# Kernel optimization log

Measured on AMD Instinct MI355X. Metric: run time of the kernel, lower is better.

## Reference

```python
import jax, jax.numpy as jnp
import numpy as np

DIM = 128
N_GNN = 3
VDW_N = 6.0
MAX_VDW = 0.0356
MIN_VDW = 0.0178
DEV_VDW_RADIUS = 0.2
DM_MIN = 0.5


def gated_gat(x, adj, W, Wb, A, gW, gb):
    # PIGNet-style GatedGAT: attention from bilinear form, gated residual
    h = x @ W + Wb                                   # [B,N,D]
    e = jnp.einsum('bjl,bkl->bjk', h @ A, h)
    e = e + jnp.swapaxes(e, 1, 2)
    att = jnp.where(adj > 0, e, -9e15)
    att = jax.nn.softmax(att, axis=-1) * adj
    hp = jax.nn.relu(jnp.einsum('bij,bjd->bid', att, h))
    coeff = jax.nn.sigmoid(jnp.concatenate([x, hp], axis=-1) @ gW + gb)  # [B,N,1]
    return coeff * x + (1.0 - coeff) * hp


def pair_mlp(lig, tgt, W1, b1, W2, b2):
    # MLP on concat([lig_i, tgt_j]) without materializing [B,L,T,2D]:
    # split W1 along its input dim (exact same math as concat @ W1)
    D = lig.shape[-1]
    pre = (jnp.einsum('bld,dk->blk', lig, W1[:D])[:, :, None, :]
           + jnp.einsum('btd,dk->btk', tgt, W1[D:])[:, None, :, :] + b1)
    h = jax.nn.relu(pre)                             # [B,L,T,D]
    return jnp.einsum('bltk,ko->blt', h, W2) + b2[0]  # [B,L,T]


def setup_inputs() -> dict:
    key = jax.random.key(0)
    ks = jax.random.split(key, 20)
    B, L, T, D = 8, 128, 512, DIM
    f32 = jnp.float32

    def adj(k, n, p):
        a = (jax.random.uniform(k, (B, n, n)) < p).astype(f32)
        a = jnp.maximum(a, jnp.swapaxes(a, 1, 2))
        return jnp.minimum(a + jnp.eye(n, dtype=f32), 1.0)

    s = 0.05
    inp = dict(
        ligand_h=jax.random.normal(ks[0], (B, L, 54), f32),
        target_h=jax.random.normal(ks[1], (B, T, 54), f32),
        ligand_adj=adj(ks[2], L, 0.10),
        target_adj=adj(ks[3], T, 0.02),
        interaction_indice=(jax.random.uniform(ks[4], (B, 3, L, T)) < 0.05).astype(f32),
        ligand_pos=jax.random.uniform(ks[5], (B, L, 3), f32) * 20.0,
        target_pos=jax.random.uniform(ks[6], (B, T, 3), f32) * 20.0,
        rotor=jnp.floor(jax.random.uniform(ks[7], (B, 1), f32) * 10.0),
        ligand_vdw_radii=jax.random.uniform(ks[8], (B, L), f32) * 0.5 + 1.5,
        target_vdw_radii=jax.random.uniform(ks[9], (B, T), f32) * 0.5 + 1.5,
        ligand_valid=jnp.ones((B, L), f32),
        target_valid=jnp.ones((B, T), f32),
        emb_W=jax.random.normal(ks[10], (54, D), f32) * s,
        gat_W=jax.random.normal(ks[11], (N_GNN, D, D), f32) * s,
        gat_Wb=jnp.zeros((N_GNN, D), f32),
        gat_A=jax.random.normal(ks[12], (N_GNN, D, D), f32) * s,
        gat_gW=jax.random.normal(ks[13], (N_GNN, 2 * D, 1), f32) * s,
        gat_gb=jnp.zeros((N_GNN, 1), f32),
        vdwA_W1=jax.random.normal(ks[14], (2 * D, D), f32) * s,
        vdwA_b1=jnp.zeros((D,), f32),
        vdwA_W2=jax.random.normal(ks[15], (D, 1), f32) * s,
        vdwA_b2=jnp.zeros((1,), f32),
        dc_W1=jax.random.normal(ks[16], (2 * D, D), f32) * s,
        dc_b1=jnp.zeros((D,), f32),
        dc_W2=jax.random.normal(ks[17], (D, 1), f32) * s,
        dc_b2=jnp.zeros((1,), f32),
        hbond_coeff=jnp.array([1.0], f32),
        metal_coeff=jnp.array([1.0], f32),
        hydrophobic_coeff=jnp.array([0.5], f32),
        rotor_coeff=jnp.array([0.5], f32),
    )
    return inp


def reference(ligand_h, target_h, ligand_adj, target_adj, interaction_indice,
              ligand_pos, target_pos, rotor, ligand_vdw_radii, target_vdw_radii,
              ligand_valid, target_valid, emb_W, gat_W, gat_Wb, gat_A, gat_gW,
              gat_gb, vdwA_W1, vdwA_b1, vdwA_W2, vdwA_b2, dc_W1, dc_b1, dc_W2,
              dc_b2, hbond_coeff, metal_coeff, hydrophobic_coeff, rotor_coeff):
    lig = ligand_h @ emb_W
    tgt = target_h @ emb_W
    # pairwise distance matrix with min-distance clamp
    diff = ligand_pos[:, :, None, :] - target_pos[:, None, :, :]
    dm = jnp.sqrt((diff * diff).sum(-1) + 1e-10)      # [B,L,T]
    dm = jnp.where(dm < DM_MIN, 1e10, dm)
    for i in range(N_GNN):  # eval mode: dropout is identity
        lig = gated_gat(lig, ligand_adj, gat_W[i], gat_Wb[i], gat_A[i], gat_gW[i], gat_gb[i])
        tgt = gated_gat(tgt, target_adj, gat_W[i], gat_Wb[i], gat_A[i], gat_gW[i], gat_gb[i])
    vdws_sum = ligand_vdw_radii[:, :, None] + target_vdw_radii[:, None, :]
    # dm_correction=True: tanh MLP on pairwise concat features, scaled by dev_vdw_radius
    vdws_sum = vdws_sum + jnp.tanh(pair_mlp(lig, tgt, dc_W1, dc_b1, dc_W2, dc_b2)) * DEV_VDW_RADIUS
    # --- vdw term ---
    dm_0 = jnp.where(vdws_sum < 1e-4, 1.0, vdws_sum)
    ratio = dm_0 / dm
    valid = ligand_valid[:, :, None] * target_valid[:, None, :]
    energy = jnp.minimum(ratio ** (2.0 * VDW_N) - 2.0 * ratio ** VDW_N, 100.0) * valid
    A = jax.nn.sigmoid(pair_mlp(lig, tgt, vdwA_W1, vdwA_b1, vdwA_W2, vdwA_b2))
    A = A * (MAX_VDW - MIN_VDW) + MIN_VDW
    vdw_e = (A * energy).sum((1, 2))                  # [B]
    # --- hbond / metal / hydrophobic ramps share dm - vdws_sum ---
    d = dm - vdws_sum
    ramp = jnp.clip(d / -0.7, 0.0, 1.0)
    hbond_e = -(hbond_coeff[0] ** 2) * (ramp * interaction_indice[:, 0]).sum((1, 2))
    metal_e = -(metal_coeff[0] ** 2) * (ramp * interaction_indice[:, 1]).sum((1, 2))
    ramp2 = jnp.clip(-d + 1.5, 0.0, 1.0)
    hydro_e = -(hydrophobic_coeff[0] ** 2) * (ramp2 * interaction_indice[:, 2]).sum((1, 2))
    energies = jnp.stack([vdw_e, hbond_e, metal_e, hydro_e], axis=-1)  # [B,4]
    energies = energies / (1.0 + rotor_coeff[0] ** 2 * rotor)          # rotor penalty
    return energies
```

## Files before the change

### kernel.cpp

```cpp
#include <hip/hip_runtime.h>
#include <hip/hip_bf16.h>
#include <math.h>

typedef __hip_bfloat16 bf16;

#define DIMD 128
#define BB 8
#define LL 128
#define TT 512

#define BMT 64
#define BKT 32
#define TGT_TILES 36
#define LIG_TILES 3

#define CV_EMBW   0L
#define CV_GATW   (CV_EMBW + 54 * 128)
#define CV_GATA   (CV_GATW + 3 * 128 * 128)
#define CV_WB     (CV_GATA + 3 * 128 * 128)
#define CV_GGW    (CV_WB + 3 * 128)
#define CV_GGB    (CV_GGW + 3 * 2 * 128)
#define CV_DCW1   (CV_GGB + 4)
#define CV_VW1    (CV_DCW1 + 2 * 128 * 128)
#define CV_TOTAL  (CV_VW1 + 2 * 128 * 128)

__device__ __forceinline__ float LD(const void* p, long i, int bf) {
    if (bf) return __bfloat162float(((const bf16*)p)[i]);
    return ((const float*)p)[i];
}

__global__ void init_cvt(const unsigned int* __restrict__ embw_raw,
                         const void* __restrict__ embW, const void* __restrict__ gatW,
                         const void* __restrict__ gatA, const void* __restrict__ gatWb,
                         const void* __restrict__ ggW, const void* __restrict__ ggb,
                         const void* __restrict__ dcW1, const void* __restrict__ vW1,
                         float* __restrict__ out, float* __restrict__ accum,
                         int* __restrict__ flagp) {
    __shared__ int cnts;
    int t = threadIdx.x;
    if (t == 0) cnts = 0;
    __syncthreads();
    unsigned int bword = (embw_raw[t] >> 8) & 0xffu;
    unsigned int e = bword & 0x7fu;
    if (e >= 0x38u && e <= 0x3fu) atomicAdd(&cnts, 1);
    __syncthreads();
    int bf = cnts > 128;
    if (blockIdx.x == 0) {
        if (t < 32) accum[t] = 0.0f;
        if (t == 0) *flagp = bf;
    }
    long i = (long)blockIdx.x * 256 + t;
    if (i >= CV_TOTAL) return;
    float v;
    if (i < CV_GATW)      v = LD(embW, i, bf);
    else if (i < CV_GATA) v = LD(gatW, i - CV_GATW, bf);
    else if (i < CV_WB)   v = LD(gatA, i - CV_GATA, bf);
    else if (i < CV_GGW)  v = LD(gatWb, i - CV_WB, bf);
    else if (i < CV_GGB)  v = LD(ggW, i - CV_GGW, bf);
    else if (i < CV_DCW1) { long j = i - CV_GGB; v = (j < 3) ? LD(ggb, j, bf) : 0.0f; }
    else if (i < CV_VW1)  v = LD(dcW1, i - CV_DCW1, bf);
    else                  v = LD(vW1, i - CV_VW1, bf);
    out[i] = v;
}

__global__ void embed_both(const void* __restrict__ Xl, const void* __restrict__ Xt,
                           const float* __restrict__ Wf, float* __restrict__ out,
                           int K, const int* __restrict__ flagp) {
    __shared__ float xrow[DIMD];
    int bf = *flagp;
    int row = blockIdx.x;
    int d = threadIdx.x;
    const void* X; long r;
    if (row < BB * LL) { X = Xl; r = row; }
    else               { X = Xt; r = row - BB * LL; }
    if (d < K) xrow[d] = LD(X, r * K + d, bf);
    __syncthreads();
    float acc = 0.0f;
    for (int k = 0; k < K; ++k)
        acc = fmaf(xrow[k], Wf[(long)k * DIMD + d], acc);
    out[(long)row * DIMD + d] = acc;
}

__global__ void gemm_hha_gate(float* __restrict__ X, const float* __restrict__ P0,
                              const float* __restrict__ P1, const float* __restrict__ cvw,
                              int layer, int dogate,
                              float* __restrict__ hout, float* __restrict__ hAout) {
    __shared__ float xs[4][DIMD];
    __shared__ float hs[4][DIMD];
    __shared__ float gred[4][2];
    long row0 = (long)blockIdx.x * 4;
    int d = threadIdx.x & 127, rg = threadIdx.x >> 7;
    int w = threadIdx.x >> 6, lane = threadIdx.x & 63;
    long r0 = row0 + rg * 2, r1 = r0 + 1;
    float xv0 = X[r0 * DIMD + d];
    float xv1 = X[r1 * DIMD + d];
    if (dogate) {
        const float* gW = cvw + CV_GGW + (long)(layer - 1) * 2 * DIMD;
        float gb = cvw[CV_GGB + (layer - 1)];
        float hp0 = fmaxf(P0[r0 * DIMD + d] + P1[r0 * DIMD + d], 0.0f);
        float hp1 = fmaxf(P0[r1 * DIMD + d] + P1[r1 * DIMD + d], 0.0f);
        float s0 = xv0 * gW[d] + hp0 * gW[DIMD + d];
        float s1 = xv1 * gW[d] + hp1 * gW[DIMD + d];
#pragma unroll
        for (int s = 32; s > 0; s >>= 1) { s0 += __shfl_xor(s0, s); s1 += __shfl_xor(s1, s); }
        if (lane == 0) { gred[rg * 2 + 0][w & 1] = s0; gred[rg * 2 + 1][w & 1] = s1; }
        __syncthreads();
        float g0 = gred[rg * 2 + 0][0] + gred[rg * 2 + 0][1] + gb;
        float g1 = gred[rg * 2 + 1][0] + gred[rg * 2 + 1][1] + gb;
        float c0 = 1.0f / (1.0f + expf(-g0));
        float c1 = 1.0f / (1.0f + expf(-g1));
        xv0 = c0 * xv0 + (1.0f - c0) * hp0;
        xv1 = c1 * xv1 + (1.0f - c1) * hp1;
        X[r0 * DIMD + d] = xv0;
        X[r1 * DIMD + d] = xv1;
    }
    xs[rg * 2 + 0][d] = xv0;
    xs[rg * 2 + 1][d] = xv1;
    __syncthreads();
    const float* W = cvw + CV_GATW + (long)layer * DIMD * DIMD;
    const float* A = cvw + CV_GATA + (long)layer * DIMD * DIMD;
    float b = cvw[CV_WB + layer * DIMD + d];
    float h0 = b, h1 = b;
    const float* x0 = xs[rg * 2];
    const float* x1 = xs[rg * 2 + 1];
#pragma unroll 8
    for (int k = 0; k < DIMD; ++k) {
        float wv = W[(long)k * DIMD + d];
        h0 = fmaf(x0[k], wv, h0);
        h1 = fmaf(x1[k], wv, h1);
    }
    long ob = r0 * DIMD + d;
    hout[ob] = h0; hout[ob + DIMD] = h1;
    hs[rg * 2][d] = h0; hs[rg * 2 + 1][d] = h1;
    __syncthreads();
    float a0 = 0.0f, a1 = 0.0f;
    const float* g0p = hs[rg * 2];
    const float* g1p = hs[rg * 2 + 1];
#pragma unroll 8
    for (int k = 0; k < DIMD; ++k) {
        float wv = A[(long)k * DIMD + d];
        a0 = fmaf(g0p[k], wv, a0);
        a1 = fmaf(g1p[k], wv, a1);
    }
    hAout[ob] = a0;
    hAout[ob + DIMD] = a1;
}

__global__ void esym_both(const float* __restrict__ hA_t, const float* __restrict__ h_t,
                          float* __restrict__ e1_t, float* __restrict__ e2_t,
                          const float* __restrict__ hA_l, const float* __restrict__ h_l,
                          float* __restrict__ e1_l, float* __restrict__ e2_l) {
    __shared__ float At[BKT][BMT + 4];
    __shared__ float Bt[BKT][BMT + 4];
    int idx = blockIdx.x, half = blockIdx.y, b = blockIdx.z, t = threadIdx.x;
    const float *hA, *h; float* e; int N;
    if (idx < TGT_TILES) { hA = hA_t; h = h_t; e = half ? e2_t : e1_t; N = TT; }
    else { idx -= TGT_TILES; hA = hA_l; h = h_l; e = half ? e2_l : e1_l; N = LL; }
    int jt = (int)((sqrtf(8.0f * idx + 1.0f) - 1.0f) * 0.5f);
    while ((jt + 1) * (jt + 2) / 2 <= idx) ++jt;
    while (jt * (jt + 1) / 2 > idx) --jt;
    int kt = idx - jt * (jt + 1) / 2;
    const float* hAb = hA + (long)b * N * DIMD;
    const float* hb  = h  + (long)b * N * DIMD;
    const float* Ap = half ? hb : hAb;
    const float* Bp = half ? hAb : hb;
    int tm = t & 15, tn = t >> 4;
    int k4 = (t & 7) * 4;
    int row0 = t >> 3;
    float acc[4][4];
#pragma unroll
    for (int i = 0; i < 4; ++i)
#pragma unroll
        for (int jj = 0; jj < 4; ++jj) acc[i][jj] = 0.0f;

#pragma unroll
    for (int c = 0; c < 4; ++c) {
        int ko = c * BKT;
        __syncthreads();
#pragma unroll
        for (int rr = 0; rr < 2; ++rr) {
            int row = row0 + rr * 32;
            float4 av = *(const float4*)&Ap[(long)(jt * BMT + row) * DIMD + ko + k4];
            float4 bv = *(const float4*)&Bp[(long)(kt * BMT + row) * DIMD + ko + k4];
            At[k4 + 0][row] = av.x; At[k4 + 1][row] = av.y;
            At[k4 + 2][row] = av.z; At[k4 + 3][row] = av.w;
            Bt[k4 + 0][row] = bv.x; Bt[k4 + 1][row] = bv.y;
            Bt[k4 + 2][row] = bv.z; Bt[k4 + 3][row] = bv.w;
        }
        __syncthreads();
#pragma unroll
        for (int k = 0; k < BKT; ++k) {
            float4 a4 = *(const float4*)&At[k][tm * 4];
            float4 b4 = *(const float4*)&Bt[k][tn * 4];
            float A[4] = {a4.x, a4.y, a4.z, a4.w};
            float Bv[4] = {b4.x, b4.y, b4.z, b4.w};
#pragma unroll
            for (int i = 0; i < 4; ++i)
#pragma unroll
                for (int jj = 0; jj < 4; ++jj)
                    acc[i][jj] = fmaf(A[i], Bv[jj], acc[i][jj]);
        }
    }
    long ebN = (long)b * N;
    long ebase = (ebN + jt * BMT + tm * 4) * N + kt * BMT + tn * 4;
#pragma unroll
    for (int i = 0; i < 4; ++i) {
        float4 v;
        v.x = acc[i][0]; v.y = acc[i][1]; v.z = acc[i][2]; v.w = acc[i][3];
        *(float4*)&e[ebase + (long)i * N] = v;
    }
    if (jt != kt) {
        long mbase = (ebN + kt * BMT + tn * 4) * N + jt * BMT + tm * 4;
#pragma unroll
        for (int jj = 0; jj < 4; ++jj) {
            float4 v;
            v.x = acc[0][jj]; v.y = acc[1][jj]; v.z = acc[2][jj]; v.w = acc[3][jj];
            *(float4*)&e[mbase + (long)jj * N] = v;
        }
    }
}

template<int CNT>
__device__ __forceinline__ void softmax_row(float* __restrict__ e1row,
                                            const float* __restrict__ e2row,
                                            const void* __restrict__ adj,
                                            long adjbase, int bf) {
    int lane = threadIdx.x & 63;
    float vals[CNT], av[CNT];
    float m = -3.4e38f;
#pragma unroll
    for (int i = 0; i < CNT; ++i) {
        int k = lane + i * 64;
        float a = LD(adj, adjbase + k, bf);
        float v = (a > 0.0f) ? (e1row[k] + e2row[k]) : -9e15f;
        av[i] = a; vals[i] = v;
        m = fmaxf(m, v);
    }
#pragma unroll
    for (int s = 32; s > 0; s >>= 1) m = fmaxf(m, __shfl_xor(m, s));
    float sum = 0.0f;
#pragma unroll
    for (int i = 0; i < CNT; ++i) { vals[i] = expf(vals[i] - m); sum += vals[i]; }
#pragma unroll
    for (int s = 32; s > 0; s >>= 1) sum += __shfl_xor(sum, s);
    float inv = 1.0f / sum;
#pragma unroll
    for (int i = 0; i < CNT; ++i)
        e1row[lane + i * 64] = vals[i] * av[i] * inv;
}

__global__ void att_softmax_both(float* __restrict__ e1_t, const float* __restrict__ e2_t,
                                 float* __restrict__ e1_l, const float* __restrict__ e2_l,
                                 const void* __restrict__ adj_t, const void* __restrict__ adj_l,
                                 const int* __restrict__ flagp) {
    int bf = *flagp;
    int b = blockIdx.y, x = blockIdx.x;
    int jr = threadIdx.x >> 6;
    if (x < TT / 4) {
        int j = x * 4 + jr;
        long base = ((long)b * TT + j) * TT;
        softmax_row<8>(e1_t + base, e2_t + base, adj_t, base, bf);
    } else {
        int j = (x - TT / 4) * 4 + jr;
        long base = ((long)b * LL + j) * LL;
        softmax_row<2>(e1_l + base, e2_l + base, adj_l, base, bf);
    }
}

__global__ void hp_gemm_both(const float* __restrict__ att_t, const float* __restrict__ h_t,
                             float* __restrict__ p0_t, float* __restrict__ p1_t,
                             const float* __restrict__ att_l, const float* __restrict__ h_l,
                             float* __restrict__ p0_l, float* __restrict__ p1_l) {
    __shared__ float At[32][36];
    __shared__ float Ht[32][DIMD];
    int jt = blockIdx.x, kc = blockIdx.y, b = blockIdx.z;
    int t = threadIdx.x;
    const float *att, *h; float *part0, *part1; int N;
    if (jt < 16) { att = att_t; h = h_t; part0 = p0_t; part1 = p1_t; N = TT; }
    else { jt -= 16; att = att_l; h = h_l; part0 = p0_l; part1 = p1_l; N = LL; }
    const float* attb = att + (long)b * N * N;
    const float* hb = h + (long)b * N * DIMD;
    int tm = t & 7, tn = t >> 3;
    float acc[4][4] = {};
    int kchunk = N / 2;
    int kbeg = kc * kchunk;
    int ar = t >> 3;
    int ac4 = (t & 7) * 4;
    int hk = t >> 5;
    int hc4 = (t & 31) * 4;
    for (int k0 = kbeg; k0 < kbeg + kchunk; k0 += 32) {
        __syncthreads();
        float4 av = *(const float4*)&attb[(long)(jt * 32 + ar) * N + k0 + ac4];
        At[ac4 + 0][ar] = av.x; At[ac4 + 1][ar] = av.y;
        At[ac4 + 2][ar] = av.z; At[ac4 + 3][ar] = av.w;
#pragma unroll
        for (int p = 0; p < 4; ++p)
            *(float4*)&Ht[hk + p * 8][hc4] = *(const float4*)&hb[(long)(k0 + hk + p * 8) * DIMD + hc4];
        __syncthreads();
#pragma unroll
        for (int k = 0; k < 32; ++k) {
            float4 a4 = *(const float4*)&At[k][tm * 4];
            float4 h4 = *(const float4*)&Ht[k][tn * 4];
            float A[4] = {a4.x, a4.y, a4.z, a4.w};
            float H[4] = {h4.x, h4.y, h4.z, h4.w};
#pragma unroll
            for (int i = 0; i < 4; ++i)
#pragma unroll
                for (int jj = 0; jj < 4; ++jj)
                    acc[i][jj] = fmaf(A[i], H[jj], acc[i][jj]);
        }
    }
    float* outp = (kc == 0) ? part0 : part1;
    long obase = ((long)b * N + jt * 32 + tm * 4) * DIMD + tn * 4;
#pragma unroll
    for (int i = 0; i < 4; ++i) {
        float4 v; v.x = acc[i][0]; v.y = acc[i][1]; v.z = acc[i][2]; v.w = acc[i][3];
        *(float4*)&outp[obase + (long)i * DIMD] = v;
    }
}

__global__ void proj_gate(const float* __restrict__ X, const float* __restrict__ P0,
                          const float* __restrict__ P1, const float* __restrict__ cvw,
                          const void* __restrict__ bdc, const void* __restrict__ bA,
                          long rowsplit, float* __restrict__ outdc, float* __restrict__ outA,
                          const int* __restrict__ flagp) {
    __shared__ float xs[4][DIMD];
    __shared__ float gred[4][2];
    int bf = *flagp;
    long row0 = (long)blockIdx.x * 4;
    int d = threadIdx.x & 127, rg = threadIdx.x >> 7;
    int w = threadIdx.x >> 6, lane = threadIdx.x & 63;
    long r0 = row0 + rg * 2, r1 = r0 + 1;
    float xv0 = X[r0 * DIMD + d];
    float xv1 = X[r1 * DIMD + d];
    {
        const float* gW = cvw + CV_GGW + 2L * 2 * DIMD;
        float gb = cvw[CV_GGB + 2];
        float hp0 = fmaxf(P0[r0 * DIMD + d] + P1[r0 * DIMD + d], 0.0f);
        float hp1 = fmaxf(P0[r1 * DIMD + d] + P1[r1 * DIMD + d], 0.0f);
        float s0 = xv0 * gW[d] + hp0 * gW[DIMD + d];
        float s1 = xv1 * gW[d] + hp1 * gW[DIMD + d];
#pragma unroll
        for (int s = 32; s > 0; s >>= 1) { s0 += __shfl_xor(s0, s); s1 += __shfl_xor(s1, s); }
        if (lane == 0) { gred[rg * 2 + 0][w & 1] = s0; gred[rg * 2 + 1][w & 1] = s1; }
        __syncthreads();
        float g0 = gred[rg * 2 + 0][0] + gred[rg * 2 + 0][1] + gb;
        float g1 = gred[rg * 2 + 1][0] + gred[rg * 2 + 1][1] + gb;
        float c0 = 1.0f / (1.0f + expf(-g0));
        float c1 = 1.0f / (1.0f + expf(-g1));
        xv0 = c0 * xv0 + (1.0f - c0) * hp0;
        xv1 = c1 * xv1 + (1.0f - c1) * hp1;
    }
    xs[rg * 2 + 0][d] = xv0;
    xs[rg * 2 + 1][d] = xv1;
    __syncthreads();
    const float* Wf = (blockIdx.y == 0) ? (cvw + CV_DCW1) : (cvw + CV_VW1);
    const void* bias = (blockIdx.y == 0) ? bdc : bA;
    float* out = (blockIdx.y == 0) ? outdc : outA;
    int sideb = row0 >= rowsplit;
    const float* W = Wf + (sideb ? (long)DIMD * DIMD : 0);
    float b0 = sideb ? 0.0f : LD(bias, d, bf);
    float a0 = b0, a1 = b0;
    const float* x0 = xs[rg * 2];
    const float* x1 = xs[rg * 2 + 1];
#pragma unroll 8
    for (int k = 0; k < DIMD; ++k) {
        float wv = W[(long)k * DIMD + d];
        a0 = fmaf(x0[k], wv, a0);
        a1 = fmaf(x1[k], wv, a1);
    }
    long ob = r0 * DIMD + d;
    out[ob] = a0;
    out[ob + DIMD] = a1;
}

__global__ void transpose_both(const float* __restrict__ in0, float* __restrict__ out0,
                               const float* __restrict__ in1, float* __restrict__ out1) {
    __shared__ float tile[32][33];
    int z = blockIdx.z;
    const float* in; float* outT; int b;
    if (z < BB) { in = in0; outT = out0; b = z; }
    else        { in = in1; outT = out1; b = z - BB; }
    int n0 = blockIdx.x * 32;
    int d0 = blockIdx.y * 32;
    int t = threadIdx.x;
    int tx = t & 31, ty = t >> 5;
    for (int r = ty; r < 32; r += 8)
        tile[r][tx] = in[((long)b * TT + n0 + r) * DIMD + d0 + tx];
    __syncthreads();
    for (int r = ty; r < 32; r += 8)
        outT[((long)b * DIMD + d0 + r) * TT + n0 + tx] = tile[tx][r];
}

__global__ void pair_energy(const float* __restrict__ ligdc, const float* __restrict__ tgtdcT,
                            const float* __restrict__ ligA, const float* __restrict__ tgtAT,
                            const void* __restrict__ dcW2, const void* __restrict__ dcb2,
                            const void* __restrict__ AW2, const void* __restrict__ Ab2,
                            const void* __restrict__ lpos, const void* __restrict__ tpos,
                            const void* __restrict__ lrad, const void* __restrict__ trad,
                            const void* __restrict__ lval, const void* __restrict__ tval,
                            const void* __restrict__ ii, float* __restrict__ accum,
                            const int* __restrict__ flagp) {
    int bf = *flagp;
    int l0 = blockIdx.x * 2, b = blockIdx.z, t = threadIdx.x;
    int tt = blockIdx.y * 256 + t;
    __shared__ __align__(16) float sdc0[DIMD], sdc1[DIMD], sA0[DIMD], sA1[DIMD];
    __shared__ __align__(16) float w2dc[DIMD], w2A[DIMD];
    __shared__ float red[256];
    if (t < DIMD) {
        sdc0[t] = ligdc[((long)b * LL + l0) * DIMD + t];
        sA0[t]  = ligA [((long)b * LL + l0) * DIMD + t];
        w2dc[t] = LD(dcW2, t, bf);
        w2A[t]  = LD(AW2, t, bf);
    } else {
        int u = t - DIMD;
        sdc1[u] = ligdc[((long)b * LL + l0 + 1) * DIMD + u];
        sA1[u]  = ligA [((long)b * LL + l0 + 1) * DIMD + u];
    }
    __syncthreads();
    const float* tdT = tgtdcT + (long)b * DIMD * TT;
    const float* taT = tgtAT  + (long)b * DIMD * TT;
    float adc0 = 0.0f, adc1 = 0.0f, aA0 = 0.0f, aA1 = 0.0f;
    for (int i4 = 0; i4 < DIMD; i4 += 4) {
#pragma unroll
        for (int j = 0; j < 4; ++j) {
            float td = tdT[(long)(i4 + j) * TT + tt];
            float ta = taT[(long)(i4 + j) * TT + tt];
            float wd = w2dc[i4 + j], wa = w2A[i4 + j];
            adc0 = fmaf(fmaxf(td + sdc0[i4 + j], 0.0f), wd, adc0);
            adc1 = fmaf(fmaxf(td + sdc1[i4 + j], 0.0f), wd, adc1);
            aA0  = fmaf(fmaxf(ta + sA0[i4 + j],  0.0f), wa, aA0);
            aA1  = fmaf(fmaxf(ta + sA1[i4 + j],  0.0f), wa, aA1);
        }
    }
    float lx0 = LD(lpos, ((long)b * LL + l0) * 3 + 0, bf);
    float ly0 = LD(lpos, ((long)b * LL + l0) * 3 + 1, bf);
    float lz0 = LD(lpos, ((long)b * LL + l0) * 3 + 2, bf);
    float lx1 = LD(lpos, ((long)b * LL + l0 + 1) * 3 + 0, bf);
    float ly1 = LD(lpos, ((long)b * LL + l0 + 1) * 3 + 1, bf);
    float lz1 = LD(lpos, ((long)b * LL + l0 + 1) * 3 + 2, bf);
    float lr0 = LD(lrad, (long)b * LL + l0, bf);
    float lr1 = LD(lrad, (long)b * LL + l0 + 1, bf);
    float lv0 = LD(lval, (long)b * LL + l0, bf);
    float lv1 = LD(lval, (long)b * LL + l0 + 1, bf);
    float cdcb2 = LD(dcb2, 0, bf), cab2 = LD(Ab2, 0, bf);
    long iiA0 = ((long)(b * 3 + 0) * LL + l0) * TT;
    long iiB0 = ((long)(b * 3 + 1) * LL + l0) * TT;
    long iiC0 = ((long)(b * 3 + 2) * LL + l0) * TT;
    long iiA1 = iiA0 + TT, iiB1 = iiB0 + TT, iiC1 = iiC0 + TT;
    float tx = LD(tpos, ((long)b * TT + tt) * 3 + 0, bf);
    float ty = LD(tpos, ((long)b * TT + tt) * 3 + 1, bf);
    float tz = LD(tpos, ((long)b * TT + tt) * 3 + 2, bf);
    float tr = LD(trad, (long)b * TT + tt, bf);
    float tv = LD(tval, (long)b * TT + tt, bf);
    float p0 = 0.0f, p1 = 0.0f, p2 = 0.0f, p3 = 0.0f;
#pragma unroll
    for (int li = 0; li < 2; ++li) {
        float dx = (li ? lx1 : lx0) - tx;
        float dy = (li ? ly1 : ly0) - ty;
        float dz = (li ? lz1 : lz0) - tz;
        float dm = sqrtf(dx * dx + dy * dy + dz * dz + 1e-10f);
        if (dm < 0.5f) dm = 1e10f;
        float adcv = li ? adc1 : adc0;
        float aAv  = li ? aA1  : aA0;
        float dev = tanhf(adcv + cdcb2) * 0.2f;
        float vdws = (li ? lr1 : lr0) + tr + dev;
        float dm0 = (vdws < 1e-4f) ? 1.0f : vdws;
        float ratio = dm0 / dm;
        float r2 = ratio * ratio, r6 = r2 * r2 * r2, r12 = r6 * r6;
        float en = fminf(r12 - 2.0f * r6, 100.0f) * (li ? lv1 : lv0) * tv;
        float As = 1.0f / (1.0f + expf(-(aAv + cab2)));
        As = As * (0.0356f - 0.0178f) + 0.0178f;
        p0 = fmaf(As, en, p0);
        float dd = dm - vdws;
        float ramp = fminf(fmaxf(dd * (1.0f / -0.7f), 0.0f), 1.0f);
        p1 = fmaf(ramp, LD(ii, (li ? iiA1 : iiA0) + tt, bf), p1);
        p2 = fmaf(ramp, LD(ii, (li ? iiB1 : iiB0) + tt, bf), p2);
        float ramp2 = fminf(fmaxf(-dd + 1.5f, 0.0f), 1.0f);
        p3 = fmaf(ramp2, LD(ii, (li ? iiC1 : iiC0) + tt, bf), p3);
    }
    for (int e = 0; e < 4; ++e) {
        float v = (e == 0) ? p0 : (e == 1) ? p1 : (e == 2) ? p2 : p3;
        red[t] = v; __syncthreads();
        for (int s = 128; s > 0; s >>= 1) { if (t < s) red[t] += red[t + s]; __syncthreads(); }
        if (t == 0) atomicAdd(&accum[b * 4 + e], red[0]);
        __syncthreads();
    }
}

__global__ void finalize(const float* __restrict__ accum, const void* __restrict__ hb,
                         const void* __restrict__ mc, const void* __restrict__ hyd,
                         const void* __restrict__ rc, const void* __restrict__ rotor,
                         void* __restrict__ out, const int* __restrict__ flagp) {
    int bf = *flagp;
    int t = threadIdx.x;
    if (t >= 32) return;
    int b = t >> 2, e = t & 3;
    float v = accum[t];
    if (e == 1) { float c = LD(hb, 0, bf);  v = -c * c * v; }
    else if (e == 2) { float c = LD(mc, 0, bf);  v = -c * c * v; }
    else if (e == 3) { float c = LD(hyd, 0, bf); v = -c * c * v; }
    float r = LD(rc, 0, bf);
    float den = 1.0f + r * r * LD(rotor, b, bf);
    float res = v / den;
    if (bf) ((bf16*)out)[t] = __float2bfloat16(res);
    else    ((float*)out)[t] = res;
}

extern "C" void kernel_launch(void* const* d_in, const int* in_sizes, int n_in,
                              void* d_out, int out_size, void* d_ws, size_t ws_size,
                              hipStream_t stream) {
    const void* ligand_h = d_in[0];
    const void* target_h = d_in[1];
    const void* ligand_adj = d_in[2];
    const void* target_adj = d_in[3];
    const void* interaction_indice = d_in[4];
    const void* ligand_pos = d_in[5];
    const void* target_pos = d_in[6];
    const void* rotor = d_in[7];
    const void* ligand_vdw = d_in[8];
    const void* target_vdw = d_in[9];
    const void* ligand_valid = d_in[10];
    const void* target_valid = d_in[11];
    const void* emb_W = d_in[12];
    const void* gat_W = d_in[13];
    const void* gat_Wb = d_in[14];
    const void* gat_A = d_in[15];
    const void* gat_gW = d_in[16];
    const void* gat_gb = d_in[17];
    const void* vdwA_W1 = d_in[18];
    const void* vdwA_b1 = d_in[19];
    const void* vdwA_W2 = d_in[20];
    const void* vdwA_b2 = d_in[21];
    const void* dc_W1 = d_in[22];
    const void* dc_b1 = d_in[23];
    const void* dc_W2 = d_in[24];
    const void* dc_b2 = d_in[25];
    const void* hbond_coeff = d_in[26];
    const void* metal_coeff = d_in[27];
    const void* hydrophobic_coeff = d_in[28];
    const void* rotor_coeff = d_in[29];

    float* ws = (float*)d_ws;
    size_t off = 0;
    float* lig_x = ws + off;  off += (size_t)BB * LL * DIMD;
    float* tgt_x = ws + off;  off += (size_t)BB * TT * DIMD;
    float* h_lig = ws + off;  off += (size_t)BB * LL * DIMD;
    float* h_tgt = ws + off;  off += (size_t)BB * TT * DIMD;
    float* hA_lig = ws + off; off += (size_t)BB * LL * DIMD;
    float* hA_tgt = ws + off; off += (size_t)BB * TT * DIMD;
    float* accum = ws + off;  off += 32;
    int* flagp = (int*)(ws + off); off += 2;
    float* e_buf = ws + off;  off += (size_t)BB * TT * TT;
    float* e_lig = ws + off;  off += (size_t)BB * LL * LL;
    float* e2_buf = ws + off; off += (size_t)BB * TT * TT;
    float* e2_lig = ws + off; off += (size_t)BB * LL * LL;
    float* part1 = ws + off;  off += (size_t)BB * (LL + TT) * DIMD;
    float* projA = ws + off;  off += (size_t)BB * (LL + TT) * DIMD;
    float* cvw   = ws + off;  off += (size_t)CV_TOTAL;
    float* part1_l = part1;
    float* part1_t = part1 + (size_t)BB * LL * DIMD;
    float* part0_lig = hA_lig;
    float* part0_tgt = hA_tgt;
    float* ligdc = h_lig;
    float* tgtdc = h_tgt;
    float* ligA = projA;
    float* tgtA = projA + (size_t)BB * LL * DIMD;
    float* tgtdcT = e_buf;
    float* tgtAT  = e_buf + (size_t)BB * DIMD * TT;
    float* wEmb = cvw + CV_EMBW;

    init_cvt<<<(CV_TOTAL + 255) / 256, 256, 0, stream>>>(
        (const unsigned int*)emb_W, emb_W, gat_W, gat_A, gat_Wb,
        gat_gW, gat_gb, dc_W1, vdwA_W1, cvw, accum, flagp);

    embed_both<<<BB * (LL + TT), DIMD, 0, stream>>>(ligand_h, target_h, wEmb, lig_x, 54, flagp);

    const long ROWSPLIT = (long)BB * LL;
    for (int i = 0; i < 3; ++i) {
        gemm_hha_gate<<<BB * (LL + TT) / 4, 256, 0, stream>>>(
            lig_x, hA_lig, part1, cvw, i, i > 0 ? 1 : 0, h_lig, hA_lig);
        esym_both<<<dim3(TGT_TILES + LIG_TILES, 2, BB), 256, 0, stream>>>(
            hA_tgt, h_tgt, e_buf, e2_buf, hA_lig, h_lig, e_lig, e2_lig);
        att_softmax_both<<<dim3(TT / 4 + LL / 4, BB), 256, 0, stream>>>(
            e_buf, e2_buf, e_lig, e2_lig, target_adj, ligand_adj, flagp);
        hp_gemm_both<<<dim3(20, 2, BB), 256, 0, stream>>>(
            e_buf, h_tgt, part0_tgt, part1_t, e_lig, h_lig, part0_lig, part1_l);
    }

    proj_gate<<<dim3(BB * (LL + TT) / 4, 2), 256, 0, stream>>>(
        lig_x, hA_lig, part1, cvw, dc_b1, vdwA_b1, ROWSPLIT, ligdc, ligA, flagp);

    transpose_both<<<dim3(TT / 32, DIMD / 32, 2 * BB), 256, 0, stream>>>(
        tgtdc, tgtdcT, tgtA, tgtAT);

    pair_energy<<<dim3(LL / 2, 2, BB), 256, 0, stream>>>(
        ligdc, tgtdcT, ligA, tgtAT, dc_W2, dc_b2, vdwA_W2, vdwA_b2,
        ligand_pos, target_pos, ligand_vdw, target_vdw,
        ligand_valid, target_valid, interaction_indice, accum, flagp);

    finalize<<<1, 64, 0, stream>>>(accum, hbond_coeff, metal_coeff,
                                   hydrophobic_coeff, rotor_coeff, rotor, d_out, flagp);
}
```

Baseline: 384.4 us.

## Split hp GEMM K four ways and restructure pair_energy tiling and reduction

The attention-times-h GEMM now splits its K dimension into four partial outputs instead of two, which doubles the grid. The gate and projection kernels sum four partials. pair_energy now has each thread handle two target columns with float2 loads and vectorised shared-memory reads, using half as many blocks. Its tree reduction through shared memory with many barriers is replaced by wave shuffles plus a small cross-wave sum. The cost is two extra partial buffers and more memory traffic when the partials are read.

```diff
diff --git a/kernel.cpp b/kernel.cpp
--- a/kernel.cpp
+++ b/kernel.cpp
@@ -82,7 +82,8 @@
 }
 
 __global__ void gemm_hha_gate(float* __restrict__ X, const float* __restrict__ P0,
-                              const float* __restrict__ P1, const float* __restrict__ cvw,
+                              const float* __restrict__ P1, const float* __restrict__ P2,
+                              const float* __restrict__ P3, const float* __restrict__ cvw,
                               int layer, int dogate,
                               float* __restrict__ hout, float* __restrict__ hAout) {
     __shared__ float xs[4][DIMD];
@@ -97,8 +98,10 @@
     if (dogate) {
         const float* gW = cvw + CV_GGW + (long)(layer - 1) * 2 * DIMD;
         float gb = cvw[CV_GGB + (layer - 1)];
-        float hp0 = fmaxf(P0[r0 * DIMD + d] + P1[r0 * DIMD + d], 0.0f);
-        float hp1 = fmaxf(P0[r1 * DIMD + d] + P1[r1 * DIMD + d], 0.0f);
+        float hp0 = fmaxf(P0[r0 * DIMD + d] + P1[r0 * DIMD + d]
+                        + P2[r0 * DIMD + d] + P3[r0 * DIMD + d], 0.0f);
+        float hp1 = fmaxf(P0[r1 * DIMD + d] + P1[r1 * DIMD + d]
+                        + P2[r1 * DIMD + d] + P3[r1 * DIMD + d], 0.0f);
         float s0 = xv0 * gW[d] + hp0 * gW[DIMD + d];
         float s1 = xv1 * gW[d] + hp1 * gW[DIMD + d];
 #pragma unroll
@@ -268,21 +271,21 @@
 }
 
 __global__ void hp_gemm_both(const float* __restrict__ att_t, const float* __restrict__ h_t,
-                             float* __restrict__ p0_t, float* __restrict__ p1_t,
                              const float* __restrict__ att_l, const float* __restrict__ h_l,
-                             float* __restrict__ p0_l, float* __restrict__ p1_l) {
+                             float* __restrict__ P0, float* __restrict__ P1,
+                             float* __restrict__ P2, float* __restrict__ P3) {
     __shared__ float At[32][36];
     __shared__ float Ht[32][DIMD];
     int jt = blockIdx.x, kc = blockIdx.y, b = blockIdx.z;
     int t = threadIdx.x;
-    const float *att, *h; float *part0, *part1; int N;
-    if (jt < 16) { att = att_t; h = h_t; part0 = p0_t; part1 = p1_t; N = TT; }
-    else { jt -= 16; att = att_l; h = h_l; part0 = p0_l; part1 = p1_l; N = LL; }
+    const float *att, *h; int N; long rowbase;
+    if (jt < 16) { att = att_t; h = h_t; N = TT; rowbase = (long)BB * LL + (long)b * TT; }
+    else { jt -= 16; att = att_l; h = h_l; N = LL; rowbase = (long)b * LL; }
     const float* attb = att + (long)b * N * N;
     const float* hb = h + (long)b * N * DIMD;
     int tm = t & 7, tn = t >> 3;
     float acc[4][4] = {};
-    int kchunk = N / 2;
+    int kchunk = N / 4;
     int kbeg = kc * kchunk;
     int ar = t >> 3;
     int ac4 = (t & 7) * 4;
@@ -310,8 +313,8 @@
                     acc[i][jj] = fmaf(A[i], H[jj], acc[i][jj]);
         }
     }
-    float* outp = (kc == 0) ? part0 : part1;
-    long obase = ((long)b * N + jt * 32 + tm * 4) * DIMD + tn * 4;
+    float* outp = (kc == 0) ? P0 : (kc == 1) ? P1 : (kc == 2) ? P2 : P3;
+    long obase = (rowbase + jt * 32 + tm * 4) * DIMD + tn * 4;
 #pragma unroll
     for (int i = 0; i < 4; ++i) {
         float4 v; v.x = acc[i][0]; v.y = acc[i][1]; v.z = acc[i][2]; v.w = acc[i][3];
@@ -320,7 +323,8 @@
 }
 
 __global__ void proj_gate(const float* __restrict__ X, const float* __restrict__ P0,
-                          const float* __restrict__ P1, const float* __restrict__ cvw,
+                          const float* __restrict__ P1, const float* __restrict__ P2,
+                          const float* __restrict__ P3, const float* __restrict__ cvw,
                           const void* __restrict__ bdc, const void* __restrict__ bA,
                           long rowsplit, float* __restrict__ outdc, float* __restrict__ outA,
                           const int* __restrict__ flagp) {
@@ -336,8 +340,10 @@
     {
         const float* gW = cvw + CV_GGW + 2L * 2 * DIMD;
         float gb = cvw[CV_GGB + 2];
-        float hp0 = fmaxf(P0[r0 * DIMD + d] + P1[r0 * DIMD + d], 0.0f);
-        float hp1 = fmaxf(P0[r1 * DIMD + d] + P1[r1 * DIMD + d], 0.0f);
+        float hp0 = fmaxf(P0[r0 * DIMD + d] + P1[r0 * DIMD + d]
+                        + P2[r0 * DIMD + d] + P3[r0 * DIMD + d], 0.0f);
+        float hp1 = fmaxf(P0[r1 * DIMD + d] + P1[r1 * DIMD + d]
+                        + P2[r1 * DIMD + d] + P3[r1 * DIMD + d], 0.0f);
         float s0 = xv0 * gW[d] + hp0 * gW[DIMD + d];
         float s1 = xv1 * gW[d] + hp1 * gW[DIMD + d];
 #pragma unroll
@@ -402,11 +408,10 @@
                             const void* __restrict__ ii, float* __restrict__ accum,
                             const int* __restrict__ flagp) {
     int bf = *flagp;
-    int l0 = blockIdx.x * 2, b = blockIdx.z, t = threadIdx.x;
-    int tt = blockIdx.y * 256 + t;
+    int l0 = blockIdx.x * 2, b = blockIdx.y, t = threadIdx.x;
     __shared__ __align__(16) float sdc0[DIMD], sdc1[DIMD], sA0[DIMD], sA1[DIMD];
     __shared__ __align__(16) float w2dc[DIMD], w2A[DIMD];
-    __shared__ float red[256];
+    __shared__ float redw[4][4];
     if (t < DIMD) {
         sdc0[t] = ligdc[((long)b * LL + l0) * DIMD + t];
         sA0[t]  = ligA [((long)b * LL + l0) * DIMD + t];
@@ -417,22 +422,27 @@
         sdc1[u] = ligdc[((long)b * LL + l0 + 1) * DIMD + u];
         sA1[u]  = ligA [((long)b * LL + l0 + 1) * DIMD + u];
     }
-    __syncthreads();
-    const float* tdT = tgtdcT + (long)b * DIMD * TT;
-    const float* taT = tgtAT  + (long)b * DIMD * TT;
-    float adc0 = 0.0f, adc1 = 0.0f, aA0 = 0.0f, aA1 = 0.0f;
-    for (int i4 = 0; i4 < DIMD; i4 += 4) {
-#pragma unroll
-        for (int j = 0; j < 4; ++j) {
-            float td = tdT[(long)(i4 + j) * TT + tt];
-            float ta = taT[(long)(i4 + j) * TT + tt];
-            float wd = w2dc[i4 + j], wa = w2A[i4 + j];
-            adc0 = fmaf(fmaxf(td + sdc0[i4 + j], 0.0f), wd, adc0);
-            adc1 = fmaf(fmaxf(td + sdc1[i4 + j], 0.0f), wd, adc1);
-            aA0  = fmaf(fmaxf(ta + sA0[i4 + j],  0.0f), wa, aA0);
-            aA1  = fmaf(fmaxf(ta + sA1[i4 + j],  0.0f), wa, aA1);
-        }
-    }
+    int tt0 = t * 2;
+    float tx0 = LD(tpos, ((long)b * TT + tt0) * 3 + 0, bf);
+    float ty0 = LD(tpos, ((long)b * TT + tt0) * 3 + 1, bf);
+    float tz0 = LD(tpos, ((long)b * TT + tt0) * 3 + 2, bf);
+    float tx1 = LD(tpos, ((long)b * TT + tt0 + 1) * 3 + 0, bf);
+    float ty1 = LD(tpos, ((long)b * TT + tt0 + 1) * 3 + 1, bf);
+    float tz1 = LD(tpos, ((long)b * TT + tt0 + 1) * 3 + 2, bf);
+    float tr0 = LD(trad, (long)b * TT + tt0, bf);
+    float tr1 = LD(trad, (long)b * TT + tt0 + 1, bf);
+    float tv0 = LD(tval, (long)b * TT + tt0, bf);
+    float tv1 = LD(tval, (long)b * TT + tt0 + 1, bf);
+    long iiA0 = ((long)(b * 3 + 0) * LL + l0) * TT;
+    long iiB0 = ((long)(b * 3 + 1) * LL + l0) * TT;
+    long iiC0 = ((long)(b * 3 + 2) * LL + l0) * TT;
+    long iiA1 = iiA0 + TT, iiB1 = iiB0 + TT, iiC1 = iiC0 + TT;
+    float iA00 = LD(ii, iiA0 + tt0, bf), iA01 = LD(ii, iiA0 + tt0 + 1, bf);
+    float iA10 = LD(ii, iiA1 + tt0, bf), iA11 = LD(ii, iiA1 + tt0 + 1, bf);
+    float iB00 = LD(ii, iiB0 + tt0, bf), iB01 = LD(ii, iiB0 + tt0 + 1, bf);
+    float iB10 = LD(ii, iiB1 + tt0, bf), iB11 = LD(ii, iiB1 + tt0 + 1, bf);
+    float iC00 = LD(ii, iiC0 + tt0, bf), iC01 = LD(ii, iiC0 + tt0 + 1, bf);
+    float iC10 = LD(ii, iiC1 + tt0, bf), iC11 = LD(ii, iiC1 + tt0 + 1, bf);
     float lx0 = LD(lpos, ((long)b * LL + l0) * 3 + 0, bf);
     float ly0 = LD(lpos, ((long)b * LL + l0) * 3 + 1, bf);
     float lz0 = LD(lpos, ((long)b * LL + l0) * 3 + 2, bf);
@@ -444,47 +454,85 @@
     float lv0 = LD(lval, (long)b * LL + l0, bf);
     float lv1 = LD(lval, (long)b * LL + l0 + 1, bf);
     float cdcb2 = LD(dcb2, 0, bf), cab2 = LD(Ab2, 0, bf);
-    long iiA0 = ((long)(b * 3 + 0) * LL + l0) * TT;
-    long iiB0 = ((long)(b * 3 + 1) * LL + l0) * TT;
-    long iiC0 = ((long)(b * 3 + 2) * LL + l0) * TT;
-    long iiA1 = iiA0 + TT, iiB1 = iiB0 + TT, iiC1 = iiC0 + TT;
-    float tx = LD(tpos, ((long)b * TT + tt) * 3 + 0, bf);
-    float ty = LD(tpos, ((long)b * TT + tt) * 3 + 1, bf);
-    float tz = LD(tpos, ((long)b * TT + tt) * 3 + 2, bf);
-    float tr = LD(trad, (long)b * TT + tt, bf);
-    float tv = LD(tval, (long)b * TT + tt, bf);
+    __syncthreads();
+    const float* tdT = tgtdcT + (long)b * DIMD * TT;
+    const float* taT = tgtAT  + (long)b * DIMD * TT;
+    float adc00 = 0.0f, adc01 = 0.0f, adc10 = 0.0f, adc11 = 0.0f;
+    float aA00 = 0.0f, aA01 = 0.0f, aA10 = 0.0f, aA11 = 0.0f;
+    for (int i4 = 0; i4 < DIMD; i4 += 4) {
+        float4 wd = *(const float4*)&w2dc[i4];
+        float4 wa = *(const float4*)&w2A[i4];
+        float4 v0d = *(const float4*)&sdc0[i4];
+        float4 v1d = *(const float4*)&sdc1[i4];
+        float4 v0a = *(const float4*)&sA0[i4];
+        float4 v1a = *(const float4*)&sA1[i4];
+        float wdv[4] = {wd.x, wd.y, wd.z, wd.w};
+        float wav[4] = {wa.x, wa.y, wa.z, wa.w};
+        float s0d[4] = {v0d.x, v0d.y, v0d.z, v0d.w};
+        float s1d[4] = {v1d.x, v1d.y, v1d.z, v1d.w};
+        float s0a[4] = {v0a.x, v0a.y, v0a.z, v0a.w};
+        float s1a[4] = {v1a.x, v1a.y, v1a.z, v1a.w};
+#pragma unroll
+        for (int j = 0; j < 4; ++j) {
+            float2 td = *(const float2*)&tdT[(long)(i4 + j) * TT + tt0];
+            float2 ta = *(const float2*)&taT[(long)(i4 + j) * TT + tt0];
+            adc00 = fmaf(fmaxf(td.x + s0d[j], 0.0f), wdv[j], adc00);
+            adc01 = fmaf(fmaxf(td.y + s0d[j], 0.0f), wdv[j], adc01);
+            adc10 = fmaf(fmaxf(td.x + s1d[j], 0.0f), wdv[j], adc10);
+            adc11 = fmaf(fmaxf(td.y + s1d[j], 0.0f), wdv[j], adc11);
+            aA00 = fmaf(fmaxf(ta.x + s0a[j], 0.0f), wav[j], aA00);
+            aA01 = fmaf(fmaxf(ta.y + s0a[j], 0.0f), wav[j], aA01);
+            aA10 = fmaf(fmaxf(ta.x + s1a[j], 0.0f), wav[j], aA10);
+            aA11 = fmaf(fmaxf(ta.y + s1a[j], 0.0f), wav[j], aA11);
+        }
+    }
     float p0 = 0.0f, p1 = 0.0f, p2 = 0.0f, p3 = 0.0f;
 #pragma unroll
-    for (int li = 0; li < 2; ++li) {
-        float dx = (li ? lx1 : lx0) - tx;
-        float dy = (li ? ly1 : ly0) - ty;
-        float dz = (li ? lz1 : lz0) - tz;
-        float dm = sqrtf(dx * dx + dy * dy + dz * dz + 1e-10f);
-        if (dm < 0.5f) dm = 1e10f;
-        float adcv = li ? adc1 : adc0;
-        float aAv  = li ? aA1  : aA0;
-        float dev = tanhf(adcv + cdcb2) * 0.2f;
-        float vdws = (li ? lr1 : lr0) + tr + dev;
-        float dm0 = (vdws < 1e-4f) ? 1.0f : vdws;
-        float ratio = dm0 / dm;
-        float r2 = ratio * ratio, r6 = r2 * r2 * r2, r12 = r6 * r6;
-        float en = fminf(r12 - 2.0f * r6, 100.0f) * (li ? lv1 : lv0) * tv;
-        float As = 1.0f / (1.0f + expf(-(aAv + cab2)));
-        As = As * (0.0356f - 0.0178f) + 0.0178f;
-        p0 = fmaf(As, en, p0);
-        float dd = dm - vdws;
-        float ramp = fminf(fmaxf(dd * (1.0f / -0.7f), 0.0f), 1.0f);
-        p1 = fmaf(ramp, LD(ii, (li ? iiA1 : iiA0) + tt, bf), p1);
-        p2 = fmaf(ramp, LD(ii, (li ? iiB1 : iiB0) + tt, bf), p2);
-        float ramp2 = fminf(fmaxf(-dd + 1.5f, 0.0f), 1.0f);
-        p3 = fmaf(ramp2, LD(ii, (li ? iiC1 : iiC0) + tt, bf), p3);
-    }
-    for (int e = 0; e < 4; ++e) {
-        float v = (e == 0) ? p0 : (e == 1) ? p1 : (e == 2) ? p2 : p3;
-        red[t] = v; __syncthreads();
-        for (int s = 128; s > 0; s >>= 1) { if (t < s) red[t] += red[t + s]; __syncthreads(); }
-        if (t == 0) atomicAdd(&accum[b * 4 + e], red[0]);
-        __syncthreads();
+    for (int jj = 0; jj < 2; ++jj) {
+        float tx = jj ? tx1 : tx0, ty = jj ? ty1 : ty0, tz = jj ? tz1 : tz0;
+        float tr = jj ? tr1 : tr0, tv = jj ? tv1 : tv0;
+#pragma unroll
+        for (int li = 0; li < 2; ++li) {
+            float dx = (li ? lx1 : lx0) - tx;
+            float dy = (li ? ly1 : ly0) - ty;
+            float dz = (li ? lz1 : lz0) - tz;
+            float dm = sqrtf(dx * dx + dy * dy + dz * dz + 1e-10f);
+            if (dm < 0.5f) dm = 1e10f;
+            float adcv = jj ? (li ? adc11 : adc01) : (li ? adc10 : adc00);
+            float aAv  = jj ? (li ? aA11  : aA01)  : (li ? aA10  : aA00);
+            float dev = tanhf(adcv + cdcb2) * 0.2f;
+            float vdws = (li ? lr1 : lr0) + tr + dev;
+            float dm0 = (vdws < 1e-4f) ? 1.0f : vdws;
+            float ratio = dm0 / dm;
+            float r2 = ratio * ratio, r6 = r2 * r2 * r2, r12 = r6 * r6;
+            float en = fminf(r12 - 2.0f * r6, 100.0f) * (li ? lv1 : lv0) * tv;
+            float As = 1.0f / (1.0f + expf(-(aAv + cab2)));
+            As = As * (0.0356f - 0.0178f) + 0.0178f;
+            p0 = fmaf(As, en, p0);
+            float dd = dm - vdws;
+            float ramp = fminf(fmaxf(dd * (1.0f / -0.7f), 0.0f), 1.0f);
+            float ramp2 = fminf(fmaxf(-dd + 1.5f, 0.0f), 1.0f);
+            float vA = jj ? (li ? iA11 : iA01) : (li ? iA10 : iA00);
+            float vB = jj ? (li ? iB11 : iB01) : (li ? iB10 : iB00);
+            float vC = jj ? (li ? iC11 : iC01) : (li ? iC10 : iC00);
+            p1 = fmaf(ramp, vA, p1);
+            p2 = fmaf(ramp, vB, p2);
+            p3 = fmaf(ramp2, vC, p3);
+        }
+    }
+#pragma unroll
+    for (int s = 32; s > 0; s >>= 1) {
+        p0 += __shfl_xor(p0, s);
+        p1 += __shfl_xor(p1, s);
+        p2 += __shfl_xor(p2, s);
+        p3 += __shfl_xor(p3, s);
+    }
+    int w = t >> 6, lane = t & 63;
+    if (lane == 0) { redw[w][0] = p0; redw[w][1] = p1; redw[w][2] = p2; redw[w][3] = p3; }
+    __syncthreads();
+    if (t < 4) {
+        float v = redw[0][t] + redw[1][t] + redw[2][t] + redw[3][t];
+        atomicAdd(&accum[b * 4 + t], v);
     }
 }
 
@@ -556,12 +604,11 @@
     float* e2_buf = ws + off; off += (size_t)BB * TT * TT;
     float* e2_lig = ws + off; off += (size_t)BB * LL * LL;
     float* part1 = ws + off;  off += (size_t)BB * (LL + TT) * DIMD;
+    float* part2 = ws + off;  off += (size_t)BB * (LL + TT) * DIMD;
+    float* part3 = ws + off;  off += (size_t)BB * (LL + TT) * DIMD;
     float* projA = ws + off;  off += (size_t)BB * (LL + TT) * DIMD;
     float* cvw   = ws + off;  off += (size_t)CV_TOTAL;
-    float* part1_l = part1;
-    float* part1_t = part1 + (size_t)BB * LL * DIMD;
-    float* part0_lig = hA_lig;
-    float* part0_tgt = hA_tgt;
+    float* part0 = hA_lig;
     float* ligdc = h_lig;
     float* tgtdc = h_tgt;
     float* ligA = projA;
@@ -579,22 +626,23 @@
     const long ROWSPLIT = (long)BB * LL;
     for (int i = 0; i < 3; ++i) {
         gemm_hha_gate<<<BB * (LL + TT) / 4, 256, 0, stream>>>(
-            lig_x, hA_lig, part1, cvw, i, i > 0 ? 1 : 0, h_lig, hA_lig);
+            lig_x, part0, part1, part2, part3, cvw, i, i > 0 ? 1 : 0, h_lig, hA_lig);
         esym_both<<<dim3(TGT_TILES + LIG_TILES, 2, BB), 256, 0, stream>>>(
             hA_tgt, h_tgt, e_buf, e2_buf, hA_lig, h_lig, e_lig, e2_lig);
         att_softmax_both<<<dim3(TT / 4 + LL / 4, BB), 256, 0, stream>>>(
             e_buf, e2_buf, e_lig, e2_lig, target_adj, ligand_adj, flagp);
-        hp_gemm_both<<<dim3(20, 2, BB), 256, 0, stream>>>(
-            e_buf, h_tgt, part0_tgt, part1_t, e_lig, h_lig, part0_lig, part1_l);
+        hp_gemm_both<<<dim3(20, 4, BB), 256, 0, stream>>>(
+            e_buf, h_tgt, e_lig, h_lig, part0, part1, part2, part3);
     }
 
     proj_gate<<<dim3(BB * (LL + TT) / 4, 2), 256, 0, stream>>>(
-        lig_x, hA_lig, part1, cvw, dc_b1, vdwA_b1, ROWSPLIT, ligdc, ligA, flagp);
+        lig_x, part0, part1, part2, part3, cvw, dc_b1, vdwA_b1, ROWSPLIT,
+        ligdc, ligA, flagp);
 
     transpose_both<<<dim3(TT / 32, DIMD / 32, 2 * BB), 256, 0, stream>>>(
         tgtdc, tgtdcT, tgtA, tgtAT);
 
-    pair_energy<<<dim3(LL / 2, 2, BB), 256, 0, stream>>>(
+    pair_energy<<<dim3(LL / 2, BB), 256, 0, stream>>>(
         ligdc, tgtdcT, ligA, tgtAT, dc_W2, dc_b2, vdwA_W2, vdwA_b2,
         ligand_pos, target_pos, ligand_vdw, target_vdw,
         ligand_valid, target_valid, interaction_indice, accum, flagp);
```

Measured after the change: 342.4 us (median of 2 runs). -10.9%, faster.
